# Kernel optimization log

Measured on AMD Instinct MI355X. Metric: run time of the kernel, lower is better.

Reference implementation:

```python
import jax, jax.numpy as jnp
import numpy as np
from jax import lax

C = 64      # channel
IMG = 21    # img_size (h = w)
D = 441     # d = IMG*IMG, odd
P = 25      # padsize = sqrt(spe_head)*sqrt(share_head) = 5*5
PS = 4      # pad_space = P - IMG
PAD1 = 220  # d // 2
START = 2   # pad_space // 2


def _unfold5(x):
    # torch nn.Unfold(kernel_size=(5,5), dilation=5) on (b, c, 25, 25) -> (b, c*25, 25)
    # input row = ph + 5*i with ph,i in [0,5): reshape rows/cols into (i, ph), (j, pw)
    b, c = x.shape[0], x.shape[1]
    xr = x.reshape(b, c, 5, 5, 5, 5)                      # (b, c, i, ph, j, pw)
    return xr.transpose(0, 1, 2, 4, 3, 5).reshape(b, c * 25, 25)


def setup_inputs() -> dict:
    key = jax.random.key(0)
    ks = jax.random.split(key, 9)
    def n(k, shape, s=0.05):
        return jax.random.normal(k, shape, dtype=jnp.float32) * s
    return {
        "x": jax.random.normal(ks[0], (2, C, IMG, IMG), dtype=jnp.float32),
        "wk": n(ks[1], (D, 1, D)),          # depthwise Conv1d weight (groups=D)
        "bk": n(ks[2], (D,)),
        "w1": n(ks[3], (25, 25, 50)),       # grouped 1x1 conv: (group, out_per_grp, in_per_grp)
        "bn_gamma": jnp.ones((25, 25), jnp.float32),
        "bn_beta": jnp.zeros((25, 25), jnp.float32),
        "bn_mean": jnp.zeros((25, 25), jnp.float32),
        "bn_var": jnp.ones((25, 25), jnp.float32),
        "w2": n(ks[4], (25, D, 25)),        # grouped 1x1 conv: (group, out_per_grp=D/..., in_per_grp)
        "b2": n(ks[5], (25, D)),
        "wv": n(ks[6], (C, 1, 3, 3)),       # depthwise 3x3 Conv2d weight
        "bv": n(ks[7], (C,)),
    }


def reference(x, wk, bk, w1, bn_gamma, bn_beta, bn_mean, bn_var, w2, b2, wv, bv):
    bs = x.shape[0]
    # key generation: depthwise conv1d over the channel axis, spatial positions as conv channels
    k = x.reshape(bs, C, IMG * IMG).transpose(0, 2, 1)    # (bs, 441, 64)
    k1 = lax.conv_general_dilated(k, wk, (1,), [(PAD1, PAD1)],
                                  dimension_numbers=("NCH", "OIH", "NCH"),
                                  feature_group_count=D) + bk[None, :, None]
    k1 = k1.transpose(0, 2, 1).reshape(bs, C, IMG, IMG)
    k1_pad = jnp.pad(k1, ((0, 0), (0, 0), (0, PS), (0, PS)))   # (bs, C, 25, 25)
    q_pad = jnp.pad(x, ((0, 0), (0, 0), (0, PS), (0, PS)))
    key_cols = _unfold5(k1_pad).transpose(0, 2, 1)             # (bs, 25, C*25)
    q_cols = _unfold5(q_pad).transpose(0, 2, 1)
    key_q = jnp.stack((q_cols, key_cols), axis=2).reshape(bs, 50, 25, C)
    kq = key_q.reshape(bs, 25, 50, C)                          # (bs, groups, in_per_grp, c)
    # attention_embed: grouped 1x1 conv -> BN(eval) -> ReLU -> grouped 1x1 conv
    att = jnp.einsum("goi,bgic->bgoc", w1, kq)                 # (bs, 25, 25, C)
    inv = bn_gamma * lax.rsqrt(bn_var + 1e-5)
    att = jax.nn.relu((att - bn_mean[None, :, :, None]) * inv[None, :, :, None]
                      + bn_beta[None, :, :, None])
    att = jnp.einsum("goi,bgic->bgoc", w2, att) + b2[None, :, :, None]   # (bs, 25, 441, C)
    att = jnp.tile(att, (1, 25, 1, 1)).transpose(0, 3, 1, 2)             # (bs, C, 625, 441)
    att = att.reshape(bs, C, 5, 5, 5, 5, D)
    att = jnp.swapaxes(att, 3, 4).reshape(bs, C, P, P, D)
    att = jax.nn.softmax(att, axis=-1).transpose(0, 1, 4, 2, 3)          # (bs, C, 441, 25, 25)
    # value path: depthwise 3x3 conv, asymmetric pad, sliding windows over channel axis
    v = lax.conv_general_dilated(x, wv, (1, 1), [(1, 1), (1, 1)],
                                 dimension_numbers=("NCHW", "OIHW", "NCHW"),
                                 feature_group_count=C) + bv[None, :, None, None]
    pad_v = jnp.pad(v, ((0, 0), (PAD1, PAD1), (PS, 0), (PS, 0)))  # (bs, 504, 25, 25)
    vf = pad_v.reshape(bs, C + D - 1, P * P)
    idx = jnp.arange(C)[:, None] + jnp.arange(D)[None, :]          # (64, 441) window indices
    vw = vf[:, idx, :].reshape(bs, C, D, P, P)
    temp = jnp.einsum("bcdhw,bcdhw->bchw", vw, att)                # multiply + sum over d
    out = temp + k1_pad
    return out[:, :, START:START + IMG, START:START + IMG]
```

## Files before the change

kernel.cpp:

```cpp
#include <hip/hip_runtime.h>

#define BVO 28224


__global__ __launch_bounds__(256) void kA(
    const float* __restrict__ x, const float* __restrict__ wk, const float* __restrict__ bk,
    const float* __restrict__ w1,
    const float* __restrict__ bn_gamma, const float* __restrict__ bn_beta,
    const float* __restrict__ bn_mean,  const float* __restrict__ bn_var,
    float* __restrict__ k1g, float* __restrict__ att1g)
{
    int blk = blockIdx.x;
    int b = blk / 25, g = blk % 25;
    int ph = g / 5, pw = g % 5;
    int tid = threadIdx.x, lane = tid & 63, wv = tid >> 6;

    __shared__ float xs[1600];
    __shared__ float k1u[1600];

    for (int u = tid; u < 1600; u += 256) {
        int c = u / 25, p = u - 25 * c;
        int row = 5*(p/5) + ph, col = 5*(p%5) + pw;
        xs[u] = (row < 21 && col < 21) ? x[b*BVO + c*441 + row*21 + col] : 0.f;
    }
    __syncthreads();

    for (int k = 0; k < 7; ++k) {
        int p = wv + 4*k;
        if (p >= 25) break;
        int row = 5*(p/5) + ph, col = 5*(p%5) + pw;
        float acc = 0.f;
        if (row < 21 && col < 21) {
            int d = row*21 + col;
            const float* wkp = wk + d*441 + 220 - lane;
            float a0 = 0.f, a1 = 0.f;
            #pragma unroll
            for (int cp = 0; cp < 64; cp += 2) {
                a0 += xs[25*cp + p]       * wkp[cp];
                a1 += xs[25*(cp+1) + p]   * wkp[cp+1];
            }
            acc = bk[d] + a0 + a1;
        }
        k1u[lane*25 + p] = acc;
        k1g[blk*1600 + p*64 + lane] = acc;
    }
    __syncthreads();

    float kq[50];
    #pragma unroll
    for (int m = 0; m < 25; ++m) kq[m] = xs[m*64 + lane];
    #pragma unroll
    for (int m = 0; m < 25; ++m) kq[25+m] = k1u[m*64 + lane];

    const float* w1g = w1 + g*1250;
    for (int k = 0; k < 7; ++k) {
        int o = wv + 4*k;
        if (o >= 25) break;
        const float* wp = w1g + o*50;
        float a0 = 0.f, a1 = 0.f;
        #pragma unroll
        for (int m = 0; m < 50; m += 2) { a0 += wp[m]*kq[m]; a1 += wp[m+1]*kq[m+1]; }
        float acc = a0 + a1;
        float inv = bn_gamma[g*25+o] * rsqrtf(bn_var[g*25+o] + 1e-5f);
        acc = (acc - bn_mean[g*25+o]) * inv + bn_beta[g*25+o];
        att1g[blk*1600 + o*64 + lane] = fmaxf(acc, 0.f);
    }
}

__global__ __launch_bounds__(256) void kB(
    const float* __restrict__ att1g, const float* __restrict__ w2,
    const float* __restrict__ b2,
    float* __restrict__ att2c, float* __restrict__ pm, float* __restrict__ pz)
{
    int blk = blockIdx.x;
    int ch = blk & 7, bg = blk >> 3;
    int g  = bg % 25;
    int tid = threadIdx.x, lane = tid & 63, wv = tid >> 6;

    float a1r[25];
    #pragma unroll
    for (int i = 0; i < 25; ++i) a1r[i] = att1g[bg*1600 + i*64 + lane];

    int base = __builtin_amdgcn_readfirstlane(56*ch + 14*wv);
    const float* w2g = w2 + g*11025 + base*25;
    const float* b2g = b2 + g*441 + base;

    float vals[14];
    #pragma unroll
    for (int j = 0; j < 14; ++j) {
        int r = base + j;
        if (r < 441) {
            const float* wp = w2g + j*25;
            float a0 = 0.f, a1 = 0.f;
            #pragma unroll
            for (int i = 0; i < 24; i += 2) { a0 += wp[i]*a1r[i]; a1 += wp[i+1]*a1r[i+1]; }
            vals[j] = b2g[j] + a0 + a1 + wp[24]*a1r[24];
            if (r >= 157 && r < 284)
                att2c[(bg*127 + (r-157))*64 + lane] = vals[j];
        } else {
            vals[j] = -1e30f;
        }
    }

    float mx = vals[0];
    #pragma unroll
    for (int j = 1; j < 14; ++j) mx = fmaxf(mx, vals[j]);

    __shared__ float red[4][64];
    red[wv][lane] = mx;
    __syncthreads();
    float M = fmaxf(fmaxf(red[0][lane], red[1][lane]), fmaxf(red[2][lane], red[3][lane]));
    float z = 0.f;
    #pragma unroll
    for (int j = 0; j < 14; ++j) z += __expf(vals[j] - M);
    __syncthreads();
    red[wv][lane] = z;
    __syncthreads();
    if (wv == 0) {
        float Z = red[0][lane] + red[1][lane] + red[2][lane] + red[3][lane];
        pm[blk*64 + lane] = M;
        pz[blk*64 + lane] = Z;
    }
}

__global__ __launch_bounds__(256) void kC(
    const float* __restrict__ x, const float* __restrict__ wvw, const float* __restrict__ bv,
    const float* __restrict__ k1g, const float* __restrict__ att2c,
    const float* __restrict__ pm, const float* __restrict__ pz,
    float* __restrict__ out)
{
    int blk = blockIdx.x;
    int b = blk / 25, g = blk % 25;
    int ph = g / 5, pw = g % 5;
    int tid = threadIdx.x, lane = tid & 63, wv = tid >> 6;

    __shared__ float a2s[8128];
    __shared__ float wT[4096];
    __shared__ float smM[64], smR[64];

    for (int i = tid; i < 8128; i += 256) a2s[i] = att2c[blk*8128 + i];
    if (tid < 64) {
        float M = -1e30f;
        #pragma unroll
        for (int c = 0; c < 8; ++c) M = fmaxf(M, pm[(blk*8 + c)*64 + tid]);
        float Z = 0.f;
        #pragma unroll
        for (int c = 0; c < 8; ++c)
            Z += pz[(blk*8 + c)*64 + tid] * __expf(pm[(blk*8 + c)*64 + tid] - M);
        smM[tid] = M;
        smR[tid] = 1.f / Z;
    }
    __syncthreads();

    float Me = smM[lane], Re = smR[lane];
    #pragma unroll
    for (int k = 0; k < 16; ++k) {
        int cv = wv + 4*k;
        wT[cv*64 + lane] = __expf(a2s[(cv + 63 - lane)*64 + lane] - Me) * Re;
    }
    __syncthreads();

    int y0 = (ph + 3) % 5, x0 = (pw + 3) % 5;
    int ny = (21 - y0 + 4) / 5, nx = (21 - x0 + 4) / 5;
    int npix = ny * nx;
    for (int k = 0; k < 7; ++k) {
        int p = wv + 4*k;
        if (p >= npix) break;
        int yy = y0 + 5*(p / nx), xx = x0 + 5*(p % nx);
        float vt = 0.f;
        if (yy >= 2 && xx >= 2) {
            int vy = yy - 2, vx = xx - 2;
            float vval = bv[lane];
            const float* xp = x + b*BVO + lane*441;
            #pragma unroll
            for (int ky = 0; ky < 3; ++ky) {
                int r2 = vy + ky - 1;
                if (r2 < 0 || r2 >= 21) continue;
                #pragma unroll
                for (int kx = 0; kx < 3; ++kx) {
                    int c2 = vx + kx - 1;
                    if (c2 < 0 || c2 >= 21) continue;
                    vval += xp[r2*21 + c2] * wvw[lane*9 + ky*3 + kx];
                }
            }
            #pragma unroll
            for (int cv = 0; cv < 64; ++cv) {
                float s = __uint_as_float(__builtin_amdgcn_readlane(__float_as_uint(vval), cv));
                vt += s * wT[cv*64 + lane];
            }
        }
        int pk = ((yy + 2 - ph) / 5) * 5 + ((xx + 2 - pw) / 5);
        float kt = k1g[blk*1600 + pk*64 + lane];
        out[b*BVO + lane*441 + yy*21 + xx] = kt + vt;
    }
}

extern "C" void kernel_launch(void* const* d_in, const int* in_sizes, int n_in,
                              void* d_out, int out_size, void* d_ws, size_t ws_size,
                              hipStream_t stream) {
    const float* x        = (const float*)d_in[0];
    const float* wk       = (const float*)d_in[1];
    const float* bk       = (const float*)d_in[2];
    const float* w1       = (const float*)d_in[3];
    const float* bn_gamma = (const float*)d_in[4];
    const float* bn_beta  = (const float*)d_in[5];
    const float* bn_mean  = (const float*)d_in[6];
    const float* bn_var   = (const float*)d_in[7];
    const float* w2       = (const float*)d_in[8];
    const float* b2       = (const float*)d_in[9];
    const float* wv       = (const float*)d_in[10];
    const float* bv       = (const float*)d_in[11];

    float* out   = (float*)d_out;
    float* k1g   = (float*)d_ws;
    float* att1g = k1g + 80000;
    float* att2c = att1g + 80000;
    float* pm    = att2c + 406400;
    float* pz    = pm + 25600;

    hipLaunchKernelGGL(kA, dim3(50), dim3(256), 0, stream,
                       x, wk, bk, w1, bn_gamma, bn_beta, bn_mean, bn_var, k1g, att1g);
    hipLaunchKernelGGL(kB, dim3(400), dim3(256), 0, stream,
                       att1g, w2, b2, att2c, pm, pz);
    hipLaunchKernelGGL(kC, dim3(50), dim3(256), 0, stream,
                       x, wv, bv, k1g, att2c, pm, pz, out);
}
```

Baseline: 38.69 us.

## Fuse three kernels into one cooperative kernel with grid sync

Replaces the three-kernel pipeline with a single cooperative launch of 400 blocks. Each block recomputes the key conv and the first grouped conv for its group, so the eight blocks sharing a group repeat that work. A grid.sync replaces the kernel boundary before the softmax-weighted value stage. The final stage spreads pixels across all 400 blocks instead of 50. This removes two launch gaps and the att1/k1 global round-trips, at the cost of redundant compute, a grid-wide barrier, and about 63KB of shared memory per block, which may limit residency.

```diff
diff --git a/kernel.cpp b/kernel.cpp
--- a/kernel.cpp
+++ b/kernel.cpp
@@ -1,7 +1,189 @@
 #include <hip/hip_runtime.h>
+#include <hip/hip_cooperative_groups.h>
+
+namespace cg = cooperative_groups;
 
 #define BVO 28224
 
+__global__ __launch_bounds__(256) void semca_coop(
+    const float* __restrict__ x, const float* __restrict__ wk, const float* __restrict__ bk,
+    const float* __restrict__ w1,
+    const float* __restrict__ bn_gamma, const float* __restrict__ bn_beta,
+    const float* __restrict__ bn_mean,  const float* __restrict__ bn_var,
+    const float* __restrict__ w2, const float* __restrict__ b2,
+    const float* __restrict__ wvw, const float* __restrict__ bv,
+    float* __restrict__ att2c, float* __restrict__ pmz,
+    float* __restrict__ out)
+{
+    cg::grid_group grid = cg::this_grid();
+
+    int blk = blockIdx.x;
+    int ch = blk & 7, bg = blk >> 3;
+    int b = bg / 25, g = bg % 25;
+    int ph = g / 5, pw = g % 5;
+    int tid = threadIdx.x, lane = tid & 63, wv = tid >> 6;
+
+    __shared__ float L[15808];
+    float* k1u  = L;
+    float* att1 = L + 1600;
+    float* red  = L + 3200;
+    float* smM  = L + 3456;
+    float* smR  = L + 3520;
+    float* zone = L + 3584;
+    float* wT   = L + 11712;
+    float* xs   = zone;
+    float* a2s  = zone;
+
+    for (int u = tid; u < 1600; u += 256) {
+        int c = u / 25, p = u - 25*c;
+        int row = 5*(p/5) + ph, col = 5*(p%5) + pw;
+        xs[u] = (row < 21 && col < 21) ? x[b*BVO + c*441 + row*21 + col] : 0.f;
+    }
+    __syncthreads();
+
+    for (int k = 0; k < 7; ++k) {
+        int p = wv + 4*k;
+        if (p >= 25) break;
+        int row = 5*(p/5) + ph, col = 5*(p%5) + pw;
+        float acc = 0.f;
+        if (row < 21 && col < 21) {
+            int d = row*21 + col;
+            const float* wkp = wk + d*441 + 220 - lane;
+            float a0 = 0.f, a1 = 0.f;
+            #pragma unroll
+            for (int cp = 0; cp < 64; cp += 2) {
+                a0 += xs[25*cp + p]     * wkp[cp];
+                a1 += xs[25*(cp+1) + p] * wkp[cp+1];
+            }
+            acc = bk[d] + a0 + a1;
+        }
+        k1u[lane*25 + p] = acc;
+    }
+    __syncthreads();
+
+    {
+        float kq[50];
+        #pragma unroll
+        for (int m = 0; m < 25; ++m) kq[m] = xs[m*64 + lane];
+        #pragma unroll
+        for (int m = 0; m < 25; ++m) kq[25+m] = k1u[m*64 + lane];
+        const float* w1g = w1 + g*1250;
+        for (int k = 0; k < 7; ++k) {
+            int o = wv + 4*k;
+            if (o >= 25) break;
+            const float* wp = w1g + o*50;
+            float a0 = 0.f, a1 = 0.f;
+            #pragma unroll
+            for (int m = 0; m < 50; m += 2) { a0 += wp[m]*kq[m]; a1 += wp[m+1]*kq[m+1]; }
+            float acc = a0 + a1;
+            float inv = bn_gamma[g*25+o] * rsqrtf(bn_var[g*25+o] + 1e-5f);
+            acc = (acc - bn_mean[g*25+o]) * inv + bn_beta[g*25+o];
+            att1[o*64 + lane] = fmaxf(acc, 0.f);
+        }
+    }
+    __syncthreads();
+
+    float a1r[25];
+    #pragma unroll
+    for (int i = 0; i < 25; ++i) a1r[i] = att1[i*64 + lane];
+
+    {
+        int base = __builtin_amdgcn_readfirstlane(56*ch + 14*wv);
+        const float* w2g = w2 + g*11025 + base*25;
+        const float* b2g = b2 + g*441 + base;
+        float vals[14];
+        #pragma unroll
+        for (int j = 0; j < 14; ++j) {
+            int r = base + j;
+            if (r < 441) {
+                const float* wp = w2g + j*25;
+                float a0 = 0.f, a1 = 0.f;
+                #pragma unroll
+                for (int i = 0; i < 24; i += 2) { a0 += wp[i]*a1r[i]; a1 += wp[i+1]*a1r[i+1]; }
+                vals[j] = b2g[j] + a0 + a1 + wp[24]*a1r[24];
+                if (r >= 157 && r < 284)
+                    att2c[(bg*127 + (r-157))*64 + lane] = vals[j];
+            } else {
+                vals[j] = -1e30f;
+            }
+        }
+        float mx = vals[0];
+        #pragma unroll
+        for (int j = 1; j < 14; ++j) mx = fmaxf(mx, vals[j]);
+        red[wv*64 + lane] = mx;
+        __syncthreads();
+        float M4 = fmaxf(fmaxf(red[0*64+lane], red[1*64+lane]),
+                         fmaxf(red[2*64+lane], red[3*64+lane]));
+        float z = 0.f;
+        #pragma unroll
+        for (int j = 0; j < 14; ++j) z += __expf(vals[j] - M4);
+        __syncthreads();
+        red[wv*64 + lane] = z;
+        __syncthreads();
+        if (wv == 0) {
+            float Z = red[0*64+lane] + red[1*64+lane] + red[2*64+lane] + red[3*64+lane];
+            pmz[blk*128 + lane]      = M4;
+            pmz[blk*128 + 64 + lane] = Z;
+        }
+    }
+
+    grid.sync();
+
+    for (int i = tid; i < 8128; i += 256) a2s[i] = att2c[bg*8128 + i];
+    if (tid < 64) {
+        float M = -1e30f;
+        #pragma unroll
+        for (int c = 0; c < 8; ++c) M = fmaxf(M, pmz[(bg*8+c)*128 + tid]);
+        float Z = 0.f;
+        #pragma unroll
+        for (int c = 0; c < 8; ++c)
+            Z += pmz[(bg*8+c)*128 + 64 + tid] * __expf(pmz[(bg*8+c)*128 + tid] - M);
+        smM[tid] = M;
+        smR[tid] = 1.f / Z;
+    }
+    __syncthreads();
+    {
+        float Me = smM[lane], Re = smR[lane];
+        #pragma unroll
+        for (int k = 0; k < 16; ++k) {
+            int cv = wv + 4*k;
+            wT[cv*64 + lane] = __expf(a2s[(cv + 63 - lane)*64 + lane] - Me) * Re;
+        }
+    }
+    __syncthreads();
+
+    int y0 = (ph + 3) % 5, x0 = (pw + 3) % 5;
+    int nx = (21 - x0 + 4) / 5, ny = (21 - y0 + 4) / 5;
+    int npix = ny * nx;
+    int p = ch + 8*wv;
+    if (p < npix) {
+        int yy = y0 + 5*(p / nx), xx = x0 + 5*(p % nx);
+        float vt = 0.f;
+        if (yy >= 2 && xx >= 2) {
+            int vy = yy - 2, vx = xx - 2;
+            float vval = bv[lane];
+            const float* xp = x + b*BVO + lane*441;
+            #pragma unroll
+            for (int ky = 0; ky < 3; ++ky) {
+                int r2 = vy + ky - 1;
+                if (r2 < 0 || r2 >= 21) continue;
+                #pragma unroll
+                for (int kx = 0; kx < 3; ++kx) {
+                    int c2 = vx + kx - 1;
+                    if (c2 < 0 || c2 >= 21) continue;
+                    vval += xp[r2*21 + c2] * wvw[lane*9 + ky*3 + kx];
+                }
+            }
+            #pragma unroll
+            for (int cv = 0; cv < 64; ++cv) {
+                float s = __uint_as_float(__builtin_amdgcn_readlane(__float_as_uint(vval), cv));
+                vt += s * wT[cv*64 + lane];
+            }
+        }
+        int pk = ((yy + 2 - ph) / 5) * 5 + ((xx + 2 - pw) / 5);
+        out[b*BVO + lane*441 + yy*21 + xx] = k1u[lane*25 + pk] + vt;
+    }
+}
 
 __global__ __launch_bounds__(256) void kA(
     const float* __restrict__ x, const float* __restrict__ wk, const float* __restrict__ bk,
@@ -14,17 +196,14 @@
     int b = blk / 25, g = blk % 25;
     int ph = g / 5, pw = g % 5;
     int tid = threadIdx.x, lane = tid & 63, wv = tid >> 6;
-
     __shared__ float xs[1600];
     __shared__ float k1u[1600];
-
     for (int u = tid; u < 1600; u += 256) {
         int c = u / 25, p = u - 25 * c;
         int row = 5*(p/5) + ph, col = 5*(p%5) + pw;
         xs[u] = (row < 21 && col < 21) ? x[b*BVO + c*441 + row*21 + col] : 0.f;
     }
     __syncthreads();
-
     for (int k = 0; k < 7; ++k) {
         int p = wv + 4*k;
         if (p >= 25) break;
@@ -36,8 +215,8 @@
             float a0 = 0.f, a1 = 0.f;
             #pragma unroll
             for (int cp = 0; cp < 64; cp += 2) {
-                a0 += xs[25*cp + p]       * wkp[cp];
-                a1 += xs[25*(cp+1) + p]   * wkp[cp+1];
+                a0 += xs[25*cp + p]     * wkp[cp];
+                a1 += xs[25*(cp+1) + p] * wkp[cp+1];
             }
             acc = bk[d] + a0 + a1;
         }
@@ -45,13 +224,11 @@
         k1g[blk*1600 + p*64 + lane] = acc;
     }
     __syncthreads();
-
     float kq[50];
     #pragma unroll
     for (int m = 0; m < 25; ++m) kq[m] = xs[m*64 + lane];
     #pragma unroll
     for (int m = 0; m < 25; ++m) kq[25+m] = k1u[m*64 + lane];
-
     const float* w1g = w1 + g*1250;
     for (int k = 0; k < 7; ++k) {
         int o = wv + 4*k;
@@ -76,15 +253,12 @@
     int ch = blk & 7, bg = blk >> 3;
     int g  = bg % 25;
     int tid = threadIdx.x, lane = tid & 63, wv = tid >> 6;
-
     float a1r[25];
     #pragma unroll
     for (int i = 0; i < 25; ++i) a1r[i] = att1g[bg*1600 + i*64 + lane];
-
     int base = __builtin_amdgcn_readfirstlane(56*ch + 14*wv);
     const float* w2g = w2 + g*11025 + base*25;
     const float* b2g = b2 + g*441 + base;
-
     float vals[14];
     #pragma unroll
     for (int j = 0; j < 14; ++j) {
@@ -101,11 +275,9 @@
             vals[j] = -1e30f;
         }
     }
-
     float mx = vals[0];
     #pragma unroll
     for (int j = 1; j < 14; ++j) mx = fmaxf(mx, vals[j]);
-
     __shared__ float red[4][64];
     red[wv][lane] = mx;
     __syncthreads();
@@ -133,11 +305,9 @@
     int b = blk / 25, g = blk % 25;
     int ph = g / 5, pw = g % 5;
     int tid = threadIdx.x, lane = tid & 63, wv = tid >> 6;
-
     __shared__ float a2s[8128];
     __shared__ float wT[4096];
     __shared__ float smM[64], smR[64];
-
     for (int i = tid; i < 8128; i += 256) a2s[i] = att2c[blk*8128 + i];
     if (tid < 64) {
         float M = -1e30f;
@@ -151,7 +321,6 @@
         smR[tid] = 1.f / Z;
     }
     __syncthreads();
-
     float Me = smM[lane], Re = smR[lane];
     #pragma unroll
     for (int k = 0; k < 16; ++k) {
@@ -159,7 +328,6 @@
         wT[cv*64 + lane] = __expf(a2s[(cv + 63 - lane)*64 + lane] - Me) * Re;
     }
     __syncthreads();
-
     int y0 = (ph + 3) % 5, x0 = (pw + 3) % 5;
     int ny = (21 - y0 + 4) / 5, nx = (21 - x0 + 4) / 5;
     int npix = ny * nx;
@@ -217,11 +385,21 @@
     float* att2c = att1g + 80000;
     float* pm    = att2c + 406400;
     float* pz    = pm + 25600;
-
-    hipLaunchKernelGGL(kA, dim3(50), dim3(256), 0, stream,
-                       x, wk, bk, w1, bn_gamma, bn_beta, bn_mean, bn_var, k1g, att1g);
-    hipLaunchKernelGGL(kB, dim3(400), dim3(256), 0, stream,
-                       att1g, w2, b2, att2c, pm, pz);
-    hipLaunchKernelGGL(kC, dim3(50), dim3(256), 0, stream,
-                       x, wv, bv, k1g, att2c, pm, pz, out);
+    float* pmz   = pz + 25600;
+
+    void* args[] = { (void*)&x, (void*)&wk, (void*)&bk, (void*)&w1,
+                     (void*)&bn_gamma, (void*)&bn_beta, (void*)&bn_mean, (void*)&bn_var,
+                     (void*)&w2, (void*)&b2, (void*)&wv, (void*)&bv,
+                     (void*)&att2c, (void*)&pmz, (void*)&out };
+    hipError_t err = hipLaunchCooperativeKernel((const void*)semca_coop,
+                                                dim3(400), dim3(256), args, 0, stream);
+    if (err != hipSuccess) {
+        (void)hipGetLastError();
+        hipLaunchKernelGGL(kA, dim3(50), dim3(256), 0, stream,
+                           x, wk, bk, w1, bn_gamma, bn_beta, bn_mean, bn_var, k1g, att1g);
+        hipLaunchKernelGGL(kB, dim3(400), dim3(256), 0, stream,
+                           att1g, w2, b2, att2c, pm, pz);
+        hipLaunchKernelGGL(kC, dim3(50), dim3(256), 0, stream,
+                           x, wv, bv, k1g, att2c, pm, pz, out);
+    }
 }
```

After: 88.36 us. 2.28x slower.

## Fuse key/attention-stage kernel into projection+softmax-stats kernel with redundant recompute

Applied to the files above, without the earlier changes.

Merges the first two kernels into one launched over 400 blocks. Each of the 8 chunk blocks for a (batch, group) pair recomputes the depthwise conv1d and the grouped 1x1 conv + BN + ReLU, and keeps att1 in shared memory instead of writing it to global memory. This removes one kernel launch and the att1 global round trip. In exchange the kA work (the wk reads and two small matmuls) is done 8 times over, and shared-memory use per block goes up.

```diff
diff --git a/kernel.cpp b/kernel.cpp
--- a/kernel.cpp
+++ b/kernel.cpp
@@ -3,23 +3,28 @@
 #define BVO 28224
 
 
-__global__ __launch_bounds__(256) void kA(
+__global__ __launch_bounds__(256) void k1k(
     const float* __restrict__ x, const float* __restrict__ wk, const float* __restrict__ bk,
     const float* __restrict__ w1,
     const float* __restrict__ bn_gamma, const float* __restrict__ bn_beta,
     const float* __restrict__ bn_mean,  const float* __restrict__ bn_var,
-    float* __restrict__ k1g, float* __restrict__ att1g)
+    const float* __restrict__ w2, const float* __restrict__ b2,
+    float* __restrict__ k1g, float* __restrict__ att2c,
+    float* __restrict__ pm, float* __restrict__ pz)
 {
     int blk = blockIdx.x;
-    int b = blk / 25, g = blk % 25;
+    int ch = blk & 7, bg = blk >> 3;
+    int b = bg / 25, g = bg % 25;
     int ph = g / 5, pw = g % 5;
     int tid = threadIdx.x, lane = tid & 63, wv = tid >> 6;
 
     __shared__ float xs[1600];
     __shared__ float k1u[1600];
+    __shared__ float att1[1600];
+    __shared__ float red[256];
 
     for (int u = tid; u < 1600; u += 256) {
-        int c = u / 25, p = u - 25 * c;
+        int c = u / 25, p = u - 25*c;
         int row = 5*(p/5) + ph, col = 5*(p%5) + pw;
         xs[u] = (row < 21 && col < 21) ? x[b*BVO + c*441 + row*21 + col] : 0.f;
     }
@@ -36,50 +41,41 @@
             float a0 = 0.f, a1 = 0.f;
             #pragma unroll
             for (int cp = 0; cp < 64; cp += 2) {
-                a0 += xs[25*cp + p]       * wkp[cp];
-                a1 += xs[25*(cp+1) + p]   * wkp[cp+1];
+                a0 += xs[25*cp + p]     * wkp[cp];
+                a1 += xs[25*(cp+1) + p] * wkp[cp+1];
             }
             acc = bk[d] + a0 + a1;
         }
         k1u[lane*25 + p] = acc;
-        k1g[blk*1600 + p*64 + lane] = acc;
-    }
-    __syncthreads();
-
-    float kq[50];
-    #pragma unroll
-    for (int m = 0; m < 25; ++m) kq[m] = xs[m*64 + lane];
-    #pragma unroll
-    for (int m = 0; m < 25; ++m) kq[25+m] = k1u[m*64 + lane];
-
-    const float* w1g = w1 + g*1250;
-    for (int k = 0; k < 7; ++k) {
-        int o = wv + 4*k;
-        if (o >= 25) break;
-        const float* wp = w1g + o*50;
-        float a0 = 0.f, a1 = 0.f;
-        #pragma unroll
-        for (int m = 0; m < 50; m += 2) { a0 += wp[m]*kq[m]; a1 += wp[m+1]*kq[m+1]; }
-        float acc = a0 + a1;
-        float inv = bn_gamma[g*25+o] * rsqrtf(bn_var[g*25+o] + 1e-5f);
-        acc = (acc - bn_mean[g*25+o]) * inv + bn_beta[g*25+o];
-        att1g[blk*1600 + o*64 + lane] = fmaxf(acc, 0.f);
-    }
-}
-
-__global__ __launch_bounds__(256) void kB(
-    const float* __restrict__ att1g, const float* __restrict__ w2,
-    const float* __restrict__ b2,
-    float* __restrict__ att2c, float* __restrict__ pm, float* __restrict__ pz)
-{
-    int blk = blockIdx.x;
-    int ch = blk & 7, bg = blk >> 3;
-    int g  = bg % 25;
-    int tid = threadIdx.x, lane = tid & 63, wv = tid >> 6;
+        if (ch == 0) k1g[bg*1600 + p*64 + lane] = acc;
+    }
+    __syncthreads();
+
+    {
+        float kq[50];
+        #pragma unroll
+        for (int m = 0; m < 25; ++m) kq[m] = xs[m*64 + lane];
+        #pragma unroll
+        for (int m = 0; m < 25; ++m) kq[25+m] = k1u[m*64 + lane];
+        const float* w1g = w1 + g*1250;
+        for (int k = 0; k < 7; ++k) {
+            int o = wv + 4*k;
+            if (o >= 25) break;
+            const float* wp = w1g + o*50;
+            float a0 = 0.f, a1 = 0.f;
+            #pragma unroll
+            for (int m = 0; m < 50; m += 2) { a0 += wp[m]*kq[m]; a1 += wp[m+1]*kq[m+1]; }
+            float acc = a0 + a1;
+            float inv = bn_gamma[g*25+o] * rsqrtf(bn_var[g*25+o] + 1e-5f);
+            acc = (acc - bn_mean[g*25+o]) * inv + bn_beta[g*25+o];
+            att1[o*64 + lane] = fmaxf(acc, 0.f);
+        }
+    }
+    __syncthreads();
 
     float a1r[25];
     #pragma unroll
-    for (int i = 0; i < 25; ++i) a1r[i] = att1g[bg*1600 + i*64 + lane];
+    for (int i = 0; i < 25; ++i) a1r[i] = att1[i*64 + lane];
 
     int base = __builtin_amdgcn_readfirstlane(56*ch + 14*wv);
     const float* w2g = w2 + g*11025 + base*25;
@@ -106,18 +102,18 @@
     #pragma unroll
     for (int j = 1; j < 14; ++j) mx = fmaxf(mx, vals[j]);
 
-    __shared__ float red[4][64];
-    red[wv][lane] = mx;
-    __syncthreads();
-    float M = fmaxf(fmaxf(red[0][lane], red[1][lane]), fmaxf(red[2][lane], red[3][lane]));
+    red[wv*64 + lane] = mx;
+    __syncthreads();
+    float M = fmaxf(fmaxf(red[0*64+lane], red[1*64+lane]),
+                    fmaxf(red[2*64+lane], red[3*64+lane]));
     float z = 0.f;
     #pragma unroll
     for (int j = 0; j < 14; ++j) z += __expf(vals[j] - M);
     __syncthreads();
-    red[wv][lane] = z;
+    red[wv*64 + lane] = z;
     __syncthreads();
     if (wv == 0) {
-        float Z = red[0][lane] + red[1][lane] + red[2][lane] + red[3][lane];
+        float Z = red[0*64+lane] + red[1*64+lane] + red[2*64+lane] + red[3*64+lane];
         pm[blk*64 + lane] = M;
         pz[blk*64 + lane] = Z;
     }
@@ -213,15 +209,13 @@
 
     float* out   = (float*)d_out;
     float* k1g   = (float*)d_ws;
-    float* att1g = k1g + 80000;
-    float* att2c = att1g + 80000;
+    float* att2c = k1g + 80000;
     float* pm    = att2c + 406400;
     float* pz    = pm + 25600;
 
-    hipLaunchKernelGGL(kA, dim3(50), dim3(256), 0, stream,
-                       x, wk, bk, w1, bn_gamma, bn_beta, bn_mean, bn_var, k1g, att1g);
-    hipLaunchKernelGGL(kB, dim3(400), dim3(256), 0, stream,
-                       att1g, w2, b2, att2c, pm, pz);
+    hipLaunchKernelGGL(k1k, dim3(400), dim3(256), 0, stream,
+                       x, wk, bk, w1, bn_gamma, bn_beta, bn_mean, bn_var,
+                       w2, b2, k1g, att2c, pm, pz);
     hipLaunchKernelGGL(kC, dim3(50), dim3(256), 0, stream,
                        x, wv, bv, k1g, att2c, pm, pz, out);
 }
```

Result: faster. 37.54 us (-3.0%).
